# Optimization experiments

Measured on AMD Instinct MI355X. Metric: run time of the kernel, lower is better.

The kernel has to match this reference:

```python
import jax, jax.numpy as jnp
import numpy as np

B, T, F, D = 2, 1, 2112, 1024
H, DH = 8, 64
INNER = H * DH
NL = 721           # cls_dim(1) + num_latents(720)
VD = 64            # vis_dim // 4
DEPTH = 6
MAX_FRAMES = 2160
EPS = 1e-5
W_SCALE = 0.02


def _ln(x, g, b):
    m = jnp.mean(x, axis=-1, keepdims=True)
    v = jnp.mean(jnp.square(x - m), axis=-1, keepdims=True)
    return (x - m) * jax.lax.rsqrt(v + EPS) * g + b


def setup_inputs() -> dict:
    key = jax.random.key(0)
    ks = jax.random.split(key, 12)
    n = lambda k, shape, s=1.0: jax.random.normal(k, shape, dtype=jnp.float32) * s
    inp = {}
    inp['x'] = n(ks[0], (B, T, F, D))
    inp['split_sizes'] = jax.random.randint(ks[1], (B,), 0, F, dtype=jnp.int32)
    # resampler parameters (randn init like torch)
    inp['latents'] = n(ks[2], (NL, D))
    inp['spatial_embs'] = n(ks[3], (VD + 1, D))
    inp['frame_embs'] = n(ks[4], (MAX_FRAMES, D))
    # per-layer attention params (stacked over depth)
    inp['nm_g'] = jnp.ones((DEPTH, D)); inp['nm_b'] = jnp.zeros((DEPTH, D))
    inp['nl_g'] = jnp.ones((DEPTH, D)); inp['nl_b'] = jnp.zeros((DEPTH, D))
    inp['wq'] = n(ks[5], (DEPTH, D, INNER), W_SCALE)
    inp['wkv'] = n(ks[6], (DEPTH, D, 2 * INNER), W_SCALE)
    inp['wo'] = n(ks[7], (DEPTH, INNER, D), W_SCALE)
    # per-layer FFN params
    inp['ffn_g'] = jnp.ones((DEPTH, D)); inp['ffn_b'] = jnp.zeros((DEPTH, D))
    inp['ffw1'] = n(ks[8], (DEPTH, D, 4 * D), W_SCALE)
    inp['ffw2'] = n(ks[9], (DEPTH, 4 * D, D), W_SCALE)
    # final norm
    inp['final_g'] = jnp.ones((D,)); inp['final_b'] = jnp.zeros((D,))
    return inp


def reference(x, split_sizes, latents, spatial_embs, frame_embs,
              nm_g, nm_b, nl_g, nl_b, wq, wkv, wo,
              ffn_g, ffn_b, ffw1, ffw2, final_g, final_b):
    b, t, f, d = x.shape
    # spatial embeddings: first VD tokens get rows [:VD], rest get row [VD] broadcast
    add_sp = jnp.concatenate(
        [spatial_embs[:VD], jnp.broadcast_to(spatial_embs[VD:VD + 1], (f - VD, d))], axis=0)
    # frame embeddings: first VD tokens get row 0, frames get rows 1..f-VD
    add_fr = jnp.concatenate(
        [jnp.broadcast_to(frame_embs[0:1], (VD, d)), frame_embs[1:f - VD + 1]], axis=0)
    x = x + (add_sp + add_fr)  # broadcast over (b, t)

    lat = jnp.broadcast_to(latents, (b, t, NL, d))

    # variable-length mask over the x part of KV; latent positions never masked
    mask_x = jnp.arange(f)[None, :] >= split_sizes[:, None]              # (b, f)
    mask = jnp.concatenate([mask_x, jnp.zeros((b, NL), dtype=bool)], -1)  # (b, f+NL)
    mask = mask[:, None, None, None, :]                                   # (b,1,1,1,j)
    scale = DH ** -0.5

    for l in range(DEPTH):
        # --- PerceiverAttention ---
        xn = _ln(x, nm_g[l], nm_b[l])
        latn = _ln(lat, nl_g[l], nl_b[l])
        q = (latn @ wq[l]).reshape(b, t, NL, H, DH) * scale
        kv = jnp.concatenate([xn, latn], axis=-2) @ wkv[l]               # (b,t,f+NL,2*inner)
        k, v = jnp.split(kv, 2, axis=-1)
        k = k.reshape(b, t, f + NL, H, DH)
        v = v.reshape(b, t, f + NL, H, DH)
        sim = jnp.einsum('btihd,btjhd->bhtij', q, k)                     # (b,h,t,NL,f+NL)
        sim = sim - jax.lax.stop_gradient(jnp.max(sim, axis=-1, keepdims=True))
        sim = jnp.where(mask, -jnp.inf, sim)
        attn = jax.nn.softmax(sim, axis=-1)
        o = jnp.einsum('bhtij,btjhd->btihd', attn, v).reshape(b, t, NL, INNER)
        lat = lat + o @ wo[l]
        # --- FeedForward ---
        h1 = _ln(lat, ffn_g[l], ffn_b[l]) @ ffw1[l]
        lat = lat + jax.nn.gelu(h1, approximate=False) @ ffw2[l]

    return _ln(lat, final_g, final_b)
```

## Files before the change

### kernel.cpp

```cpp
#include <hip/hip_runtime.h>
#include <math.h>

constexpr int B = 2;
constexpr int F = 2112;
constexpr int D = 1024;
constexpr int H = 8;
constexpr int DH = 64;
constexpr int INNER = H * DH;
constexpr int NL = 721;
constexpr int NL_PAD = 768;
constexpr int MLAT = B * NL;
constexpr int MLAT_PAD = 1536;
constexpr int VD = 64;
constexpr int DEPTH = 6;
constexpr int FN = F + NL;
constexpr int FN_PAD = 2880;
constexpr int NBH = B * H;
constexpr int SKVMAX = 8;
constexpr int MX = B * F;
constexpr int NBIAS = 6656;
constexpr float EPS = 1e-5f;

typedef __bf16 bf16x8 __attribute__((ext_vector_type(8)));
typedef float  f32x4  __attribute__((ext_vector_type(4)));

static __device__ __forceinline__ unsigned short f2bf(float f)
{
    union { float f; unsigned int u; } x; x.f = f;
    unsigned int r = x.u + 0x7FFFu + ((x.u >> 16) & 1u);
    return (unsigned short)(r >> 16);
}
static __device__ __forceinline__ float bf2f(unsigned short u)
{
    union { unsigned int i; float f; } x; x.i = ((unsigned int)u) << 16; return x.f;
}

static __device__ __forceinline__ int xcd_swz(int b, int nt)
{
    return (b & 7) * (nt >> 3) + (b >> 3);
}

__device__ __forceinline__ void block_reduce_2(float& s, float& ss, float* red)
{
#pragma unroll
    for (int off = 32; off; off >>= 1) {
        s  += __shfl_xor(s, off);
        ss += __shfl_xor(ss, off);
    }
    int wv = threadIdx.x >> 6;
    if ((threadIdx.x & 63) == 0) { red[wv] = s; red[4 + wv] = ss; }
    __syncthreads();
    s  = red[0] + red[1] + red[2] + red[3];
    ss = red[4] + red[5] + red[6] + red[7];
}

__global__ __launch_bounds__(256) void emb_ln_kernel(
    const float* __restrict__ x, const float* __restrict__ sp_emb,
    const float* __restrict__ fr_emb, unsigned short* __restrict__ xhat)
{
    __shared__ float red[8];
    int r = blockIdx.x;
    int j = r % F;
    int t = threadIdx.x;
    const float4* xr = (const float4*)(x + (long)r * D);
    int spr = (j < VD) ? j : VD;
    int frr = (j < VD) ? 0 : (j - VD + 1);
    const float4* sp4 = (const float4*)(sp_emb + (long)spr * D);
    const float4* fr4 = (const float4*)(fr_emb + (long)frr * D);
    float4 v = xr[t], a = sp4[t], c = fr4[t];
    v.x += a.x + c.x; v.y += a.y + c.y; v.z += a.z + c.z; v.w += a.w + c.w;
    float s  = v.x + v.y + v.z + v.w;
    float ss = v.x*v.x + v.y*v.y + v.z*v.z + v.w*v.w;
    block_reduce_2(s, ss, red);
    float mean = s * (1.0f / D);
    float var  = ss * (1.0f / D) - mean * mean;
    float rstd = rsqrtf(var + EPS);
    ushort4 o;
    o.x = f2bf((v.x - mean) * rstd);
    o.y = f2bf((v.y - mean) * rstd);
    o.z = f2bf((v.z - mean) * rstd);
    o.w = f2bf((v.w - mean) * rstd);
    ((ushort4*)(xhat + (long)r * D))[t] = o;
}

__global__ __launch_bounds__(256) void rownorm_plain_kernel(
    const float* __restrict__ in, unsigned short* __restrict__ out)
{
    __shared__ float red[8];
    int r = blockIdx.x;
    int t = threadIdx.x;
    float4 v = ((const float4*)(in + (long)r * D))[t];
    float s  = v.x + v.y + v.z + v.w;
    float ss = v.x*v.x + v.y*v.y + v.z*v.z + v.w*v.w;
    block_reduce_2(s, ss, red);
    float mean = s * (1.0f / D);
    float var  = ss * (1.0f / D) - mean * mean;
    float rstd = rsqrtf(var + EPS);
    ushort4 o;
    o.x = f2bf((v.x - mean) * rstd);
    o.y = f2bf((v.y - mean) * rstd);
    o.z = f2bf((v.z - mean) * rstd);
    o.w = f2bf((v.w - mean) * rstd);
    ((ushort4*)(out + (long)r * D))[t] = o;
}

__global__ __launch_bounds__(256) void final_ln_kernel(
    const float* __restrict__ in, const float* __restrict__ g,
    const float* __restrict__ b, float* __restrict__ out)
{
    __shared__ float red[8];
    int r = blockIdx.x;
    int t = threadIdx.x;
    float4 v = ((const float4*)(in + (long)r * D))[t];
    float s  = v.x + v.y + v.z + v.w;
    float ss = v.x*v.x + v.y*v.y + v.z*v.z + v.w*v.w;
    block_reduce_2(s, ss, red);
    float mean = s * (1.0f / D);
    float var  = ss * (1.0f / D) - mean * mean;
    float rstd = rsqrtf(var + EPS);
    float4 g4 = ((const float4*)g)[t];
    float4 b4 = ((const float4*)b)[t];
    float4 o;
    o.x = (v.x - mean) * rstd * g4.x + b4.x;
    o.y = (v.y - mean) * rstd * g4.y + b4.y;
    o.z = (v.z - mean) * rstd * g4.z + b4.z;
    o.w = (v.w - mean) * rstd * g4.w + b4.w;
    ((float4*)(out + (long)r * D))[t] = o;
}

__global__ __launch_bounds__(256) void lat_init_kernel(
    const float* __restrict__ latents, float* __restrict__ lat)
{
    int r = blockIdx.x;
    int i = r % NL;
    int t = threadIdx.x;
    ((float4*)(lat + (long)r * D))[t] = ((const float4*)(latents + (long)i * D))[t];
}

__global__ __launch_bounds__(256) void bias_kernel(
    const float* __restrict__ wq, const float* __restrict__ wkv,
    const float* __restrict__ ffw1,
    const float* __restrict__ nl_b, const float* __restrict__ nm_b,
    const float* __restrict__ ffn_b, float* __restrict__ bias)
{
    int l = blockIdx.z;
    int o = blockIdx.x * 256 + threadIdx.x;
    int k0 = blockIdx.y * 128;
    const float* W; const float* bv; int n, Nd;
    if (o < 512)       { W = wq   + (long)l * D * INNER;     bv = nl_b  + (long)l * D; n = o;        Nd = INNER; }
    else if (o < 1536) { W = wkv  + (long)l * D * 2 * INNER; bv = nl_b  + (long)l * D; n = o - 512;  Nd = 2 * INNER; }
    else if (o < 2560) { W = wkv  + (long)l * D * 2 * INNER; bv = nm_b  + (long)l * D; n = o - 1536; Nd = 2 * INNER; }
    else               { W = ffw1 + (long)l * D * 4 * D;     bv = ffn_b + (long)l * D; n = o - 2560; Nd = 4 * D; }
    float s = 0.f;
#pragma unroll 4
    for (int k = k0; k < k0 + 128; ++k)
        s += bv[k] * W[(long)k * Nd + n];
    unsafeAtomicAdd(&bias[(long)l * NBIAS + o], s);
}

constexpr long WL_LAT = 1536L * 1024;
constexpr long WL_KVX = 1024L * 1024;
constexpr long WL_WO  = 1024L * 512;
constexpr long WL_F1  = 4096L * 1024;
constexpr long WL_F2  = 1024L * 4096;
constexpr long WL_SZ  = WL_LAT + WL_KVX + WL_WO + WL_F1 + WL_F2;

__device__ __forceinline__ void conv_tile128(
    const float* __restrict__ src, unsigned short* __restrict__ dst,
    int Kd, int Nd, int tn, int tk, const float* __restrict__ g, float* lds)
{
    int t = threadIdx.x;
    int n0 = tn * 64, k0 = tk * 128;
#pragma unroll
    for (int p = 0; p < 32; ++p) {
        int idx = p * 256 + t;
        int kr = idx >> 6, nc = idx & 63;
        float val = src[(long)(k0 + kr) * Nd + n0 + nc];
        if (g) val *= g[k0 + kr];
        lds[nc * 129 + kr] = val;
    }
    __syncthreads();
#pragma unroll
    for (int p = 0; p < 4; ++p) {
        int nr = p * 16 + (t >> 4);
        int kc = t & 15;
        unsigned short u[8];
#pragma unroll
        for (int j = 0; j < 8; ++j)
            u[j] = f2bf(lds[nr * 129 + kc * 8 + j]);
        *(uint4*)(dst + (long)(n0 + nr) * Kd + k0 + kc * 8) = *(uint4*)u;
    }
}

__global__ __launch_bounds__(256) void wt_conv_all_kernel(
    const float* __restrict__ wq, const float* __restrict__ wkv,
    const float* __restrict__ wo, const float* __restrict__ ffw1,
    const float* __restrict__ ffw2,
    const float* __restrict__ nl_g, const float* __restrict__ nm_g,
    const float* __restrict__ ffn_g,
    unsigned short* __restrict__ wbuf, long wstride, int layer0)
{
    __shared__ float lds[64 * 129];
    int l = layer0 + blockIdx.y;
    unsigned short* wl = wbuf + (long)blockIdx.y * wstride;
    const float* wq_l   = wq   + (long)l * D * INNER;
    const float* wkv_l  = wkv  + (long)l * D * 2 * INNER;
    const float* wo_l   = wo   + (long)l * INNER * D;
    const float* ffw1_l = ffw1 + (long)l * D * 4 * D;
    const float* ffw2_l = ffw2 + (long)l * 4 * D * D;
    const float* nlg = nl_g + (long)l * D;
    const float* nmg = nm_g + (long)l * D;
    const float* ffg = ffn_g + (long)l * D;

    int T = blockIdx.x;
    if (T < 64) {
        conv_tile128(wq_l, wl, D, INNER, T & 7, T >> 3, nlg, lds);
    } else if (T < 192) {
        int Ti = T - 64;
        conv_tile128(wkv_l, wl + 512L * D, D, 2 * INNER, Ti & 15, Ti >> 4, nlg, lds);
    } else if (T < 320) {
        int Ti = T - 192;
        conv_tile128(wkv_l, wl + WL_LAT, D, 2 * INNER, Ti & 15, Ti >> 4, nmg, lds);
    } else if (T < 384) {
        int Ti = T - 320;
        conv_tile128(wo_l, wl + WL_LAT + WL_KVX, INNER, D, Ti & 15, Ti >> 4, nullptr, lds);
    } else if (T < 896) {
        int Ti = T - 384;
        conv_tile128(ffw1_l, wl + WL_LAT + WL_KVX + WL_WO, D, 4 * D, Ti & 63, Ti >> 6, ffg, lds);
    } else {
        int Ti = T - 896;
        conv_tile128(ffw2_l, wl + WL_LAT + WL_KVX + WL_WO + WL_F1, 4 * D, D, Ti & 15, Ti >> 4, nullptr, lds);
    }
}

__device__ __forceinline__ void load_set(
    const unsigned short* __restrict__ ap, const unsigned short* __restrict__ bp,
    long rs, int ko, bf16x8 (&av)[4], bf16x8 (&bv)[4])
{
#pragma unroll
    for (int q = 0; q < 4; ++q) {
        av[q] = *(const bf16x8*)(ap + q * rs + ko);
        bv[q] = *(const bf16x8*)(bp + q * rs + ko);
    }
}

__device__ __forceinline__ void mfma_set(
    const bf16x8 (&av)[4], const bf16x8 (&bv)[4], f32x4 (&acc)[4][4])
{
#pragma unroll
    for (int mm = 0; mm < 4; ++mm)
#pragma unroll
        for (int nn = 0; nn < 4; ++nn)
            acc[mm][nn] = __builtin_amdgcn_mfma_f32_16x16x32_bf16(av[mm], bv[nn], acc[mm][nn], 0, 0, 0);
}

__device__ __forceinline__ void gemm_core(
    const unsigned short* __restrict__ ap, const unsigned short* __restrict__ bp,
    long rs, int Kc, f32x4 (&acc)[4][4])
{
    bf16x8 aC[4], bC[4], aN[4], bN[4];
    load_set(ap, bp, rs, 0, aC, bC);
    for (int ko = 0; ko < Kc; ko += 64) {
        load_set(ap, bp, rs, ko + 32, aN, bN);
        mfma_set(aC, bC, acc);
        if (ko + 64 < Kc)
            load_set(ap, bp, rs, ko + 64, aC, bC);
        mfma_set(aN, bN, acc);
    }
}

__global__ __launch_bounds__(64) void qkv_fused_kernel(
    const unsigned short* __restrict__ la, const unsigned short* __restrict__ xhat,
    const unsigned short* __restrict__ wlatT, const float* __restrict__ bias_l,
    unsigned short* __restrict__ qb, unsigned short* __restrict__ kb,
    unsigned short* __restrict__ vt)
{
    int lane = threadIdx.x;
    int lr = lane & 15, lg = lane >> 4;

    const unsigned short* A;
    const unsigned short* Bt;
    long m0, n0;
    int M, rpb, joff, qcols;
    bool isLat;
    int T = xcd_swz(blockIdx.x, 1608);
    if (T < 552) {
        int bm = T % 23, bn = T / 23;
        A = la; Bt = wlatT;
        m0 = (long)bm * 64; n0 = (long)bn * 64;
        M = MLAT; rpb = NL; joff = F; qcols = 512; isLat = true;
    } else {
        int Ti = T - 552;
        int bm = Ti % 66, bn = Ti / 66;
        A = xhat; Bt = wlatT + WL_LAT;
        m0 = (long)bm * 64; n0 = (long)bn * 64;
        M = MX; rpb = F; joff = 0; qcols = 0; isLat = false;
    }

    const unsigned short* ap = A  + (m0 + lr) * D + lg * 8;
    const unsigned short* bp = Bt + (n0 + lr) * D + lg * 8;
    f32x4 acc[4][4] = {};
    gemm_core(ap, bp, 16L * D, D, acc);

#pragma unroll
    for (int mm = 0; mm < 4; ++mm) {
        long ar0 = m0 + mm * 16 + lg * 4;
        if (ar0 >= M) continue;
#pragma unroll
        for (int nn = 0; nn < 4; ++nn) {
            long col = n0 + nn * 16 + lr;
            float bcol = isLat ? bias_l[col] : bias_l[1536 + col];
            f32x4 v = acc[mm][nn];
#pragma unroll
            for (int r = 0; r < 4; ++r) v[r] += bcol;
            if (col < qcols) {
#pragma unroll
                for (int r = 0; r < 4; ++r) {
                    long ar = ar0 + r;
                    if (ar < M) {
                        int bb = ar >= NL;
                        long i = ar - (bb ? NL : 0);
                        qb[((long)bb * NL_PAD + i) * INNER + col] = f2bf(v[r] * 0.125f);
                    }
                }
            } else {
                int c = (int)col - qcols;
                if (c < 512) {
#pragma unroll
                    for (int r = 0; r < 4; ++r) {
                        long ar = ar0 + r;
                        if (ar < M) {
                            int bb = ar >= rpb;
                            long i = ar - (bb ? rpb : 0);
                            kb[((long)bb * FN_PAD + joff + i) * INNER + c] = f2bf(v[r]);
                        }
                    }
                } else {
                    int d = c - 512;
                    int bb0 = ar0 >= rpb;
                    int bb3 = (ar0 + 3) >= rpb;
                    long i0 = ar0 - (bb0 ? rpb : 0);
                    long j0 = joff + i0;
                    if ((ar0 + 3 < M) && (bb0 == bb3) && ((j0 & 3) == 0)) {
                        ushort4 pk;
                        pk.x = f2bf(v[0]); pk.y = f2bf(v[1]);
                        pk.z = f2bf(v[2]); pk.w = f2bf(v[3]);
                        *(ushort4*)(vt + ((long)bb0 * INNER + d) * FN_PAD + j0) = pk;
                    } else {
#pragma unroll
                        for (int r = 0; r < 4; ++r) {
                            long ar = ar0 + r;
                            if (ar < M) {
                                int bb = ar >= rpb;
                                long i = ar - (bb ? rpb : 0);
                                vt[((long)bb * INNER + d) * FN_PAD + joff + i] = f2bf(v[r]);
                            }
                        }
                    }
                }
            }
        }
    }
}

#define MODE_RESA  0
#define MODE_GELU  1

__global__ __launch_bounds__(64) void gemm_split_kernel(
    const unsigned short* __restrict__ A, const unsigned short* __restrict__ Bt,
    void* __restrict__ C, const float* __restrict__ bias,
    int M, int K, int Kc, int mode, int ldc, int bmN, int bnN)
{
    int lane = threadIdx.x;
    int lr = lane & 15, lg = lane >> 4;
    int u = xcd_swz(blockIdx.x, gridDim.x);
    int bm = u % bmN;
    int t2 = u / bmN;
    int bn = t2 % bnN;
    int kz = t2 / bnN;
    long m0 = (long)bm * 64;
    long n0 = (long)bn * 64;
    int k0 = kz * Kc;

    const unsigned short* ap = A  + (m0 + lr) * K + k0 + lg * 8;
    const unsigned short* bp = Bt + (n0 + lr) * K + k0 + lg * 8;
    f32x4 acc[4][4] = {};
    gemm_core(ap, bp, 16L * K, Kc, acc);

#pragma unroll
    for (int mm = 0; mm < 4; ++mm) {
        long ar0 = m0 + mm * 16 + lg * 4;
        if (ar0 >= M) continue;
#pragma unroll
        for (int nn = 0; nn < 4; ++nn) {
            long col = n0 + nn * 16 + lr;
            f32x4 v = acc[mm][nn];
            if (mode == MODE_RESA) {
                float* p = (float*)C;
#pragma unroll
                for (int r = 0; r < 4; ++r)
                    if (ar0 + r < M)
                        unsafeAtomicAdd(&p[(ar0 + r) * (long)ldc + col], v[r]);
            } else {
                float bcol = bias ? bias[col] : 0.f;
                unsigned short* p = (unsigned short*)C;
#pragma unroll
                for (int r = 0; r < 4; ++r)
                    if (ar0 + r < M) {
                        float val = v[r] + bcol;
                        val = 0.5f * val * (1.0f + erff(val * 0.70710678118654752f));
                        p[(ar0 + r) * (long)ldc + col] = f2bf(val);
                    }
            }
        }
    }
}

__global__ __launch_bounds__(256) void attn_split_kernel(
    const unsigned short* __restrict__ qb, const unsigned short* __restrict__ kb,
    const unsigned short* __restrict__ vt, const int* __restrict__ split,
    float* __restrict__ po, float* __restrict__ pml, int skv)
{
    int u = xcd_swz(blockIdx.x, gridDim.x);
    int q64  = u % 12;
    int bh   = (u / 12) % NBH;
    int sidx = u / (12 * NBH);
    int b  = bh >> 3;
    int h  = bh & 7;
    int w  = threadIdx.x >> 6;
    int lane = threadIdx.x & 63;
    int q0 = q64 * 64 + w * 16;
    if (q0 >= NL) return;

    __shared__ unsigned short p_lds[4][16 * 64];
    unsigned short* pl = p_lds[w];

    int lr = lane & 15;
    int lg = lane >> 4;

    bf16x8 qa0, qa1;
    {
        const unsigned short* qrow = qb + ((long)b * NL_PAD + q0 + lr) * INNER + h * 64;
        qa0 = *(const bf16x8*)(qrow + lg * 8);
        qa1 = *(const bf16x8*)(qrow + 32 + lg * 8);
    }

    f32x4 oacc[4] = {{0,0,0,0},{0,0,0,0},{0,0,0,0},{0,0,0,0}};
    float m[4]    = {-1e30f, -1e30f, -1e30f, -1e30f};
    float lsum[4] = {0.f, 0.f, 0.f, 0.f};

    int sp = split[b];
    if (sp < 0) sp = 0;
    if (sp > F) sp = F;
    int ntx = (sp + 63) >> 6;
    int ntot = ntx + 12;
    int t0 = (ntot * sidx) / skv;
    int t1 = (ntot * (sidx + 1)) / skv;

    for (int t = t0; t < t1; ++t) {
        int j0, limit;
        if (t < ntx) { j0 = t * 64;             limit = sp; }
        else         { j0 = F + (t - ntx) * 64; limit = FN; }

        f32x4 s[4] = {{0,0,0,0},{0,0,0,0},{0,0,0,0},{0,0,0,0}};
        const unsigned short* kbase =
            kb + ((long)b * FN_PAD + j0 + lr) * INNER + h * 64 + lg * 8;
#pragma unroll
        for (int st = 0; st < 4; ++st) {
            bf16x8 kf0 = *(const bf16x8*)(kbase + (long)st * 16 * INNER);
            bf16x8 kf1 = *(const bf16x8*)(kbase + (long)st * 16 * INNER + 32);
            s[st] = __builtin_amdgcn_mfma_f32_16x16x32_bf16(qa0, kf0, s[st], 0, 0, 0);
            s[st] = __builtin_amdgcn_mfma_f32_16x16x32_bf16(qa1, kf1, s[st], 0, 0, 0);
        }

        if (j0 + 64 > limit) {
#pragma unroll
            for (int st = 0; st < 4; ++st) {
                bool valid = (j0 + st * 16 + lr) < limit;
#pragma unroll
                for (int r = 0; r < 4; ++r)
                    s[st][r] = valid ? s[st][r] : -1e30f;
            }
        }

        float tm[4];
#pragma unroll
        for (int r = 0; r < 4; ++r)
            tm[r] = fmaxf(fmaxf(s[0][r], s[1][r]), fmaxf(s[2][r], s[3][r]));
#pragma unroll
        for (int off = 1; off < 16; off <<= 1) {
#pragma unroll
            for (int r = 0; r < 4; ++r)
                tm[r] = fmaxf(tm[r], __shfl_xor(tm[r], off));
        }
        float cr[4];
#pragma unroll
        for (int r = 0; r < 4; ++r) {
            float mn = fmaxf(m[r], tm[r]);
            cr[r] = __expf(m[r] - mn);
            m[r]  = mn;
        }
#pragma unroll
        for (int st = 0; st < 4; ++st)
#pragma unroll
            for (int r = 0; r < 4; ++r)
                s[st][r] = __expf(s[st][r] - m[r]);
        float ts[4];
#pragma unroll
        for (int r = 0; r < 4; ++r)
            ts[r] = (s[0][r] + s[1][r]) + (s[2][r] + s[3][r]);
#pragma unroll
        for (int off = 1; off < 16; off <<= 1) {
#pragma unroll
            for (int r = 0; r < 4; ++r)
                ts[r] += __shfl_xor(ts[r], off);
        }
#pragma unroll
        for (int r = 0; r < 4; ++r)
            lsum[r] = lsum[r] * cr[r] + ts[r];
#pragma unroll
        for (int nst = 0; nst < 4; ++nst)
#pragma unroll
            for (int r = 0; r < 4; ++r)
                oacc[nst][r] *= cr[r];

#pragma unroll
        for (int st = 0; st < 4; ++st)
#pragma unroll
            for (int r = 0; r < 4; ++r) {
                int row  = lg * 4 + r;
                int col  = st * 16 + lr;
                int byte = (row * 128 + col * 2) ^ ((row & 7) << 4);
                *(unsigned short*)((char*)pl + byte) = f2bf(s[st][r]);
            }

#pragma unroll
        for (int kk = 0; kk < 2; ++kk) {
            int row  = lr;
            int byte = (row * 128 + kk * 64 + lg * 16) ^ ((row & 7) << 4);
            bf16x8 pa = *(const bf16x8*)((char*)pl + byte);
#pragma unroll
            for (int nst = 0; nst < 4; ++nst) {
                const unsigned short* vp =
                    vt + ((long)bh * DH + nst * 16 + lr) * FN_PAD + j0 + kk * 32 + lg * 8;
                bf16x8 vf = *(const bf16x8*)vp;
                oacc[nst] = __builtin_amdgcn_mfma_f32_16x16x32_bf16(pa, vf, oacc[nst], 0, 0, 0);
            }
        }
    }

    long base = ((long)sidx * NBH + bh) * NL_PAD;
#pragma unroll
    for (int nst = 0; nst < 4; ++nst)
#pragma unroll
        for (int r = 0; r < 4; ++r) {
            int row = q0 + lg * 4 + r;
            if (row < NL)
                po[(base + row) * DH + nst * 16 + lr] = oacc[nst][r];
        }
    if (lr == 0) {
#pragma unroll
        for (int r = 0; r < 4; ++r) {
            int row = q0 + lg * 4 + r;
            if (row < NL) {
                pml[(base + row) * 2 + 0] = m[r];
                pml[(base + row) * 2 + 1] = lsum[r];
            }
        }
    }
}

__global__ __launch_bounds__(256) void attn_combine_kernel(
    const float* __restrict__ po, const float* __restrict__ pml,
    unsigned short* __restrict__ o, int skv)
{
    int row = blockIdx.x * 4 + (threadIdx.x >> 6);
    if (row >= NBH * NL) return;
    int lane = threadIdx.x & 63;
    int bh = row / NL;
    int i  = row - bh * NL;
    int b = bh >> 3, h = bh & 7;

    float m = -1e30f, l = 0.0f, acc = 0.0f;
    for (int s = 0; s < skv; ++s) {
        long base = ((long)s * NBH + bh) * NL_PAD + i;
        float ms = pml[base * 2 + 0];
        float ls = pml[base * 2 + 1];
        float os = po[base * DH + lane];
        float mn = fmaxf(m, ms);
        float c1 = __expf(m - mn);
        float c2 = __expf(ms - mn);
        acc = acc * c1 + os * c2;
        l   = l * c1 + ls * c2;
        m   = mn;
    }
    o[((long)b * NL + i) * INNER + h * 64 + lane] = f2bf(acc / l);
}

extern "C" void kernel_launch(void* const* d_in, const int* in_sizes, int n_in,
                              void* d_out, int out_size, void* d_ws, size_t ws_size,
                              hipStream_t stream)
{
    const float* x        = (const float*)d_in[0];
    const int*   split    = (const int*)d_in[1];
    const float* latents  = (const float*)d_in[2];
    const float* sp_emb   = (const float*)d_in[3];
    const float* fr_emb   = (const float*)d_in[4];
    const float* nm_g     = (const float*)d_in[5];
    const float* nm_b     = (const float*)d_in[6];
    const float* nl_g     = (const float*)d_in[7];
    const float* nl_b     = (const float*)d_in[8];
    const float* wq       = (const float*)d_in[9];
    const float* wkv      = (const float*)d_in[10];
    const float* wo       = (const float*)d_in[11];
    const float* ffn_g    = (const float*)d_in[12];
    const float* ffn_b    = (const float*)d_in[13];
    const float* ffw1     = (const float*)d_in[14];
    const float* ffw2     = (const float*)d_in[15];
    const float* final_g  = (const float*)d_in[16];
    const float* final_b  = (const float*)d_in[17];
    float* out = (float*)d_out;

    char* cur = (char*)d_ws;
    auto alloc = [&](size_t bytes) {
        void* p = (void*)cur;
        cur += (bytes + 255) & ~(size_t)255;
        return p;
    };

    unsigned short* xhat = (unsigned short*)alloc((long)MX * D * 2);
    float* lat  = (float*)alloc((long)B * NL * D * 4);
    unsigned short* la  = (unsigned short*)alloc((long)MLAT_PAD * D * 2);
    unsigned short* fa  = (unsigned short*)alloc((long)MLAT_PAD * D * 2);
    unsigned short* h1b = (unsigned short*)alloc((long)MLAT_PAD * 4 * D * 2);
    unsigned short* ob  = (unsigned short*)alloc((long)MLAT_PAD * INNER * 2);
    unsigned short* qb  = (unsigned short*)alloc((long)B * NL_PAD * INNER * 2);
    unsigned short* kb  = (unsigned short*)alloc((long)B * FN_PAD * INNER * 2);
    unsigned short* vt  = (unsigned short*)alloc((long)B * FN_PAD * INNER * 2);
    float* bias = (float*)alloc((long)DEPTH * NBIAS * 4);
    float* pml  = (float*)alloc((long)SKVMAX * NBH * NL_PAD * 2 * 4);

    size_t fixed = (size_t)(cur - (char*)d_ws);
    const size_t po8 = ((size_t)8 * NBH * NL_PAD * DH * 4 + 255) & ~(size_t)255;
    const size_t po4 = ((size_t)4 * NBH * NL_PAD * DH * 4 + 255) & ~(size_t)255;
    const size_t wb6 = ((size_t)6 * WL_SZ * 2 + 255) & ~(size_t)255;
    const size_t wb1 = ((size_t)WL_SZ * 2 + 255) & ~(size_t)255;
    const size_t margin = 4096;

    int skv;
    bool hoist_w;
    if (fixed + po8 + wb6 + margin <= ws_size)      { skv = 8; hoist_w = true;  }
    else if (fixed + po4 + wb6 + margin <= ws_size) { skv = 4; hoist_w = true;  }
    else if (fixed + po8 + wb1 + margin <= ws_size) { skv = 8; hoist_w = false; }
    else                                            { skv = 4; hoist_w = false; }

    float* po = (float*)alloc(skv == 8 ? po8 : po4);
    unsigned short* wbuf = (unsigned short*)alloc(hoist_w ? wb6 : wb1);

    hipMemsetAsync(bias, 0, (size_t)DEPTH * NBIAS * 4, stream);

    emb_ln_kernel<<<MX, 256, 0, stream>>>(x, sp_emb, fr_emb, xhat);
    lat_init_kernel<<<B * NL, 256, 0, stream>>>(latents, lat);
    bias_kernel<<<dim3(NBIAS / 256, 8, 6), 256, 0, stream>>>(
        wq, wkv, ffw1, nl_b, nm_b, ffn_b, bias);

    if (hoist_w)
        wt_conv_all_kernel<<<dim3(1408, 6), 256, 0, stream>>>(
            wq, wkv, wo, ffw1, ffw2, nl_g, nm_g, ffn_g, wbuf, WL_SZ, 0);

    for (int l = 0; l < DEPTH; ++l) {
        unsigned short* wl = wbuf + (hoist_w ? (long)l * WL_SZ : 0);
        if (!hoist_w)
            wt_conv_all_kernel<<<dim3(1408, 1), 256, 0, stream>>>(
                wq, wkv, wo, ffw1, ffw2, nl_g, nm_g, ffn_g, wbuf, 0, l);

        unsigned short* wlatT = wl;
        unsigned short* woT   = wl + WL_LAT + WL_KVX;
        unsigned short* f1T   = wl + WL_LAT + WL_KVX + WL_WO;
        unsigned short* f2T   = wl + WL_LAT + WL_KVX + WL_WO + WL_F1;
        const float* bias_l = bias + (long)l * NBIAS;

        rownorm_plain_kernel<<<MLAT, 256, 0, stream>>>(lat, la);

        qkv_fused_kernel<<<1608, 64, 0, stream>>>(la, xhat, wlatT, bias_l, qb, kb, vt);

        attn_split_kernel<<<12 * NBH * skv, 256, 0, stream>>>(
            qb, kb, vt, split, po, pml, skv);
        attn_combine_kernel<<<(NBH * NL + 3) / 4, 256, 0, stream>>>(po, pml, ob, skv);

        gemm_split_kernel<<<23 * 16 * 4, 64, 0, stream>>>(
            ob, woT, lat, nullptr, MLAT, INNER, 128, MODE_RESA, D, 23, 16);

        rownorm_plain_kernel<<<MLAT, 256, 0, stream>>>(lat, fa);
        gemm_split_kernel<<<23 * 64, 64, 0, stream>>>(
            fa, f1T, h1b, bias_l + 2560, MLAT, D, D, MODE_GELU, 4 * D, 23, 64);
        gemm_split_kernel<<<23 * 16 * 8, 64, 0, stream>>>(
            h1b, f2T, lat, MLAT ? nullptr : nullptr, MLAT, 4 * D, 512, MODE_RESA, D, 23, 16);
    }

    final_ln_kernel<<<MLAT, 256, 0, stream>>>(lat, final_g, final_b, out);
}
```

Measured before the change: 1.901 ms.

## Split K across two waves in QKV and FFN1 GEMMs, halve weight-conversion tiles

The QKV and FFN1-GELU GEMMs now run two wavefronts per block, each covering half of K, and combine partial accumulators through LDS before the epilogue. This doubles the waves per output tile, which raises occupancy and shortens each wave's serial K loop for these long-K GEMMs. The weight conversion kernel uses 64x64 tiles instead of 128x64, doubling the block count and reducing LDS per block. The cost is an extra LDS reduction and barrier per tile, and the second wave sits idle during the epilogue.

```diff
diff --git a/kernel.cpp b/kernel.cpp
--- a/kernel.cpp
+++ b/kernel.cpp
@@ -165,30 +165,30 @@
 constexpr long WL_F2  = 1024L * 4096;
 constexpr long WL_SZ  = WL_LAT + WL_KVX + WL_WO + WL_F1 + WL_F2;
 
-__device__ __forceinline__ void conv_tile128(
+__device__ __forceinline__ void conv_tile64(
     const float* __restrict__ src, unsigned short* __restrict__ dst,
     int Kd, int Nd, int tn, int tk, const float* __restrict__ g, float* lds)
 {
     int t = threadIdx.x;
-    int n0 = tn * 64, k0 = tk * 128;
-#pragma unroll
-    for (int p = 0; p < 32; ++p) {
+    int n0 = tn * 64, k0 = tk * 64;
+#pragma unroll
+    for (int p = 0; p < 16; ++p) {
         int idx = p * 256 + t;
         int kr = idx >> 6, nc = idx & 63;
         float val = src[(long)(k0 + kr) * Nd + n0 + nc];
         if (g) val *= g[k0 + kr];
-        lds[nc * 129 + kr] = val;
+        lds[nc * 65 + kr] = val;
     }
     __syncthreads();
 #pragma unroll
-    for (int p = 0; p < 4; ++p) {
-        int nr = p * 16 + (t >> 4);
-        int kc = t & 15;
+    for (int p = 0; p < 2; ++p) {
+        int nl_ = p * 32 + (t >> 3);
+        int kc  = t & 7;
         unsigned short u[8];
 #pragma unroll
         for (int j = 0; j < 8; ++j)
-            u[j] = f2bf(lds[nr * 129 + kc * 8 + j]);
-        *(uint4*)(dst + (long)(n0 + nr) * Kd + k0 + kc * 8) = *(uint4*)u;
+            u[j] = f2bf(lds[nl_ * 65 + kc * 8 + j]);
+        *(uint4*)(dst + (long)(n0 + nl_) * Kd + k0 + kc * 8) = *(uint4*)u;
     }
 }
 
@@ -200,7 +200,7 @@
     const float* __restrict__ ffn_g,
     unsigned short* __restrict__ wbuf, long wstride, int layer0)
 {
-    __shared__ float lds[64 * 129];
+    __shared__ float lds[64 * 65];
     int l = layer0 + blockIdx.y;
     unsigned short* wl = wbuf + (long)blockIdx.y * wstride;
     const float* wq_l   = wq   + (long)l * D * INNER;
@@ -213,23 +213,23 @@
     const float* ffg = ffn_g + (long)l * D;
 
     int T = blockIdx.x;
-    if (T < 64) {
-        conv_tile128(wq_l, wl, D, INNER, T & 7, T >> 3, nlg, lds);
-    } else if (T < 192) {
-        int Ti = T - 64;
-        conv_tile128(wkv_l, wl + 512L * D, D, 2 * INNER, Ti & 15, Ti >> 4, nlg, lds);
-    } else if (T < 320) {
-        int Ti = T - 192;
-        conv_tile128(wkv_l, wl + WL_LAT, D, 2 * INNER, Ti & 15, Ti >> 4, nmg, lds);
+    if (T < 128) {
+        conv_tile64(wq_l, wl, D, INNER, T & 7, T >> 3, nlg, lds);
     } else if (T < 384) {
-        int Ti = T - 320;
-        conv_tile128(wo_l, wl + WL_LAT + WL_KVX, INNER, D, Ti & 15, Ti >> 4, nullptr, lds);
-    } else if (T < 896) {
+        int Ti = T - 128;
+        conv_tile64(wkv_l, wl + 512L * D, D, 2 * INNER, Ti & 15, Ti >> 4, nlg, lds);
+    } else if (T < 640) {
         int Ti = T - 384;
-        conv_tile128(ffw1_l, wl + WL_LAT + WL_KVX + WL_WO, D, 4 * D, Ti & 63, Ti >> 6, ffg, lds);
+        conv_tile64(wkv_l, wl + WL_LAT, D, 2 * INNER, Ti & 15, Ti >> 4, nmg, lds);
+    } else if (T < 768) {
+        int Ti = T - 640;
+        conv_tile64(wo_l, wl + WL_LAT + WL_KVX, INNER, D, Ti & 15, Ti >> 4, nullptr, lds);
+    } else if (T < 1792) {
+        int Ti = T - 768;
+        conv_tile64(ffw1_l, wl + WL_LAT + WL_KVX + WL_WO, D, 4 * D, Ti & 63, Ti >> 6, ffg, lds);
     } else {
-        int Ti = T - 896;
-        conv_tile128(ffw2_l, wl + WL_LAT + WL_KVX + WL_WO + WL_F1, 4 * D, D, Ti & 15, Ti >> 4, nullptr, lds);
+        int Ti = T - 1792;
+        conv_tile64(ffw2_l, wl + WL_LAT + WL_KVX + WL_WO + WL_F1, 4 * D, D, Ti & 15, Ti >> 4, nullptr, lds);
     }
 }
 
@@ -269,13 +269,41 @@
     }
 }
 
-__global__ __launch_bounds__(64) void qkv_fused_kernel(
+__device__ __forceinline__ bool ksplit_reduce(
+    f32x4 (&acc)[4][4], float* red, int w, int lg, int lr)
+{
+    if (w == 1) {
+#pragma unroll
+        for (int mm = 0; mm < 4; ++mm)
+#pragma unroll
+            for (int nn = 0; nn < 4; ++nn)
+#pragma unroll
+                for (int r = 0; r < 4; ++r)
+                    red[(mm * 16 + lg * 4 + r) * 65 + nn * 16 + lr] = acc[mm][nn][r];
+    }
+    __syncthreads();
+    if (w == 0) {
+#pragma unroll
+        for (int mm = 0; mm < 4; ++mm)
+#pragma unroll
+            for (int nn = 0; nn < 4; ++nn)
+#pragma unroll
+                for (int r = 0; r < 4; ++r)
+                    acc[mm][nn][r] += red[(mm * 16 + lg * 4 + r) * 65 + nn * 16 + lr];
+        return true;
+    }
+    return false;
+}
+
+__global__ __launch_bounds__(128) void qkv_fused_kernel(
     const unsigned short* __restrict__ la, const unsigned short* __restrict__ xhat,
     const unsigned short* __restrict__ wlatT, const float* __restrict__ bias_l,
     unsigned short* __restrict__ qb, unsigned short* __restrict__ kb,
     unsigned short* __restrict__ vt)
 {
-    int lane = threadIdx.x;
+    __shared__ float red[64 * 65];
+    int tid = threadIdx.x;
+    int w = tid >> 6, lane = tid & 63;
     int lr = lane & 15, lg = lane >> 4;
 
     const unsigned short* A;
@@ -297,10 +325,12 @@
         M = MX; rpb = F; joff = 0; qcols = 0; isLat = false;
     }
 
-    const unsigned short* ap = A  + (m0 + lr) * D + lg * 8;
-    const unsigned short* bp = Bt + (n0 + lr) * D + lg * 8;
+    const unsigned short* ap = A  + (m0 + lr) * D + w * 512 + lg * 8;
+    const unsigned short* bp = Bt + (n0 + lr) * D + w * 512 + lg * 8;
     f32x4 acc[4][4] = {};
-    gemm_core(ap, bp, 16L * D, D, acc);
+    gemm_core(ap, bp, 16L * D, 512, acc);
+
+    if (!ksplit_reduce(acc, red, w, lg, lr)) return;
 
 #pragma unroll
     for (int mm = 0; mm < 4; ++mm) {
@@ -363,13 +393,50 @@
     }
 }
 
-#define MODE_RESA  0
-#define MODE_GELU  1
+__global__ __launch_bounds__(128) void gemm_gelu2_kernel(
+    const unsigned short* __restrict__ A, const unsigned short* __restrict__ Bt,
+    unsigned short* __restrict__ C, const float* __restrict__ bias,
+    int M, int K, int ldc, int bmN)
+{
+    __shared__ float red[64 * 65];
+    int tid = threadIdx.x;
+    int w = tid >> 6, lane = tid & 63;
+    int lr = lane & 15, lg = lane >> 4;
+    int u = xcd_swz(blockIdx.x, gridDim.x);
+    int bm = u % bmN, bn = u / bmN;
+    long m0 = (long)bm * 64, n0 = (long)bn * 64;
+    int kh = K >> 1;
+
+    const unsigned short* ap = A  + (m0 + lr) * K + w * kh + lg * 8;
+    const unsigned short* bp = Bt + (n0 + lr) * K + w * kh + lg * 8;
+    f32x4 acc[4][4] = {};
+    gemm_core(ap, bp, 16L * K, kh, acc);
+
+    if (!ksplit_reduce(acc, red, w, lg, lr)) return;
+
+#pragma unroll
+    for (int mm = 0; mm < 4; ++mm) {
+        long ar0 = m0 + mm * 16 + lg * 4;
+        if (ar0 >= M) continue;
+#pragma unroll
+        for (int nn = 0; nn < 4; ++nn) {
+            long col = n0 + nn * 16 + lr;
+            float bcol = bias[col];
+            f32x4 v = acc[mm][nn];
+#pragma unroll
+            for (int r = 0; r < 4; ++r)
+                if (ar0 + r < M) {
+                    float val = v[r] + bcol;
+                    val = 0.5f * val * (1.0f + erff(val * 0.70710678118654752f));
+                    C[(ar0 + r) * (long)ldc + col] = f2bf(val);
+                }
+        }
+    }
+}
 
 __global__ __launch_bounds__(64) void gemm_split_kernel(
     const unsigned short* __restrict__ A, const unsigned short* __restrict__ Bt,
-    void* __restrict__ C, const float* __restrict__ bias,
-    int M, int K, int Kc, int mode, int ldc, int bmN, int bnN)
+    float* __restrict__ C, int M, int K, int Kc, int ldc, int bmN, int bnN)
 {
     int lane = threadIdx.x;
     int lr = lane & 15, lg = lane >> 4;
@@ -395,23 +462,10 @@
         for (int nn = 0; nn < 4; ++nn) {
             long col = n0 + nn * 16 + lr;
             f32x4 v = acc[mm][nn];
-            if (mode == MODE_RESA) {
-                float* p = (float*)C;
-#pragma unroll
-                for (int r = 0; r < 4; ++r)
-                    if (ar0 + r < M)
-                        unsafeAtomicAdd(&p[(ar0 + r) * (long)ldc + col], v[r]);
-            } else {
-                float bcol = bias ? bias[col] : 0.f;
-                unsigned short* p = (unsigned short*)C;
-#pragma unroll
-                for (int r = 0; r < 4; ++r)
-                    if (ar0 + r < M) {
-                        float val = v[r] + bcol;
-                        val = 0.5f * val * (1.0f + erff(val * 0.70710678118654752f));
-                        p[(ar0 + r) * (long)ldc + col] = f2bf(val);
-                    }
-            }
+#pragma unroll
+            for (int r = 0; r < 4; ++r)
+                if (ar0 + r < M)
+                    unsafeAtomicAdd(&C[(ar0 + r) * (long)ldc + col], v[r]);
         }
     }
 }
@@ -665,13 +719,13 @@
         wq, wkv, ffw1, nl_b, nm_b, ffn_b, bias);
 
     if (hoist_w)
-        wt_conv_all_kernel<<<dim3(1408, 6), 256, 0, stream>>>(
+        wt_conv_all_kernel<<<dim3(2816, 6), 256, 0, stream>>>(
             wq, wkv, wo, ffw1, ffw2, nl_g, nm_g, ffn_g, wbuf, WL_SZ, 0);
 
     for (int l = 0; l < DEPTH; ++l) {
         unsigned short* wl = wbuf + (hoist_w ? (long)l * WL_SZ : 0);
         if (!hoist_w)
-            wt_conv_all_kernel<<<dim3(1408, 1), 256, 0, stream>>>(
+            wt_conv_all_kernel<<<dim3(2816, 1), 256, 0, stream>>>(
                 wq, wkv, wo, ffw1, ffw2, nl_g, nm_g, ffn_g, wbuf, 0, l);
 
         unsigned short* wlatT = wl;
@@ -682,20 +736,20 @@
 
         rownorm_plain_kernel<<<MLAT, 256, 0, stream>>>(lat, la);
 
-        qkv_fused_kernel<<<1608, 64, 0, stream>>>(la, xhat, wlatT, bias_l, qb, kb, vt);
+        qkv_fused_kernel<<<1608, 128, 0, stream>>>(la, xhat, wlatT, bias_l, qb, kb, vt);
 
         attn_split_kernel<<<12 * NBH * skv, 256, 0, stream>>>(
             qb, kb, vt, split, po, pml, skv);
         attn_combine_kernel<<<(NBH * NL + 3) / 4, 256, 0, stream>>>(po, pml, ob, skv);
 
         gemm_split_kernel<<<23 * 16 * 4, 64, 0, stream>>>(
-            ob, woT, lat, nullptr, MLAT, INNER, 128, MODE_RESA, D, 23, 16);
+            ob, woT, lat, MLAT, INNER, 128, D, 23, 16);
 
         rownorm_plain_kernel<<<MLAT, 256, 0, stream>>>(lat, fa);
-        gemm_split_kernel<<<23 * 64, 64, 0, stream>>>(
-            fa, f1T, h1b, bias_l + 2560, MLAT, D, D, MODE_GELU, 4 * D, 23, 64);
+        gemm_gelu2_kernel<<<23 * 64, 128, 0, stream>>>(
+            fa, f1T, h1b, bias_l + 2560, MLAT, D, 4 * D, 23);
         gemm_split_kernel<<<23 * 16 * 8, 64, 0, stream>>>(
-            h1b, f2T, lat, MLAT ? nullptr : nullptr, MLAT, 4 * D, 512, MODE_RESA, D, 23, 16);
+            h1b, f2T, lat, MLAT, 4 * D, 512, D, 23, 16);
     }
 
     final_ln_kernel<<<MLAT, 256, 0, stream>>>(lat, final_g, final_b, out);
```

Result: no change. 1.907 ms (+0.3%).
